# Kernel tuning notes

Hardware: AMD Instinct MI355X
Metric: run time of the kernel (lower is better)

Reference implementation:

```python
import jax, jax.numpy as jnp
import numpy as np

K = 8            # top-k neighbors per channel
BN_EPS = 1e-3    # keras BatchNormalization default


def top_k_features(h, adj, k):
    # h: [N, F], adj: [N, N] (dense). Per node and per channel, take the k
    # largest masked neighbor feature values, then prepend the node's own feature.
    masked = adj[:, None, :] * h.T[None, :, :]        # [N, F, N]
    topk = jax.lax.top_k(masked, k)[0]                # [N, F, K]
    topk = jnp.transpose(topk, (0, 2, 1))             # [N, K, F]
    return jnp.concatenate([h[:, None, :], topk], axis=1)  # [N, K+1, F]


def conv1d(x, w):
    # x: [N, L, Cin], w: [kw, Cin, Cout], VALID 1D conv
    return jax.lax.conv_general_dilated(x, w, (1,), 'VALID',
                                        dimension_numbers=('NWC', 'WIO', 'NWC'))


def batchnorm(x, gamma, beta, mean, var):
    return gamma * (x - mean) * jax.lax.rsqrt(var + BN_EPS) + beta


def setup_inputs():
    key = jax.random.key(0)
    ks = jax.random.split(key, 16)
    N, Fin, H, Cout, NF = 1600, 1433, 32, 7, 8
    x = jax.random.normal(ks[0], (N, Fin), jnp.float32)
    # sparse binary adjacency, avg degree ~16
    adj = (jax.random.uniform(ks[1], (N, N)) < 0.01).astype(jnp.float32)
    mask = jax.random.uniform(ks[2], (N,)) < 0.5

    def g(k, shape, fan_in):
        return jax.random.normal(k, shape, jnp.float32) * (1.0 / np.sqrt(fan_in))

    W0 = g(ks[3], (Fin, H), Fin)                 # DenseConvolution (GCN) weight
    # LGConv block 1: F=32 -> mid (32+8)//2=20 -> 8; kernels 5,5 reduce 9->5->1
    W1a = g(ks[4], (5, 32, 20), 5 * 32)
    W1b = g(ks[5], (5, 20, NF), 5 * 20)
    # LGConv block 2: F=40 -> mid (40+8)//2=24 -> 8
    W2a = g(ks[6], (5, 40, 24), 5 * 40)
    W2b = g(ks[7], (5, 24, NF), 5 * 24)
    Wout = g(ks[8], (H + 2 * NF, Cout), H + 2 * NF)  # 48 -> 7
    bn = {}
    for i, kk in ((1, 9), (2, 12)):
        bn[f'g{i}'] = 1.0 + 0.1 * jax.random.normal(ks[kk], (NF,), jnp.float32)
        bn[f'b{i}'] = 0.1 * jax.random.normal(ks[kk + 1], (NF,), jnp.float32)
        bn[f'm{i}'] = 0.1 * jax.random.normal(ks[kk + 2], (NF,), jnp.float32)
        bn[f'v{i}'] = jax.random.uniform(ks[kk], (NF,), jnp.float32, 0.5, 1.5)
    return {'x': x, 'adj': adj, 'W0': W0, 'W1a': W1a, 'W1b': W1b,
            'W2a': W2a, 'W2b': W2b, 'Wout': Wout,
            'g1': bn['g1'], 'b1': bn['b1'], 'm1': bn['m1'], 'v1': bn['v1'],
            'g2': bn['g2'], 'b2': bn['b2'], 'm2': bn['m2'], 'v2': bn['v2'],
            'mask': mask}


def reference(x, adj, W0, W1a, W1b, W2a, W2b, Wout,
              g1, b1, m1, v1, g2, b2, m2, v2, mask):
    # inference mode: dropout = identity
    h = adj @ (x @ W0)                                # GCN layer, hidden=32
    for Wa, Wb, g, b, m, v in ((W1a, W1b, g1, b1, m1, v1),
                               (W2a, W2b, g2, b2, m2, v2)):
        t = top_k_features(h, adj, K)                 # [N, K+1, F]
        c = conv1d(t, Wa)                             # [N, 5, mid]
        c = conv1d(c, Wb)[:, 0, :]                    # [N, 8]
        c = batchnorm(c, g, b, m, v)
        h = jnp.concatenate([h, c], axis=-1)          # 32 -> 40 -> 48
    logits = adj @ (h @ Wout)                         # [N, 7]
    # Mask layer (boolean_mask); static-shape variant: zero out masked rows
    return jnp.where(mask[:, None], logits, 0.0)
```

## Files before the change

kernel.cpp:

```cpp
#include <hip/hip_runtime.h>


constexpr int NN   = 1600;
constexpr int FIN  = 1433;
constexpr int HGCN = 32;
constexpr int NBS  = 96;
constexpr float BN_EPS = 1e-3f;

constexpr int KS    = 16;
constexpr int CHUNK = 90;
constexpr int BM    = 32;
constexpr int SXS   = 92;
constexpr int RB    = NN / BM;
constexpr int CSRB  = 400;
constexpr int K1B   = CSRB + 1 + RB * KS;
constexpr int GB    = 256;
constexpr int NT    = 512;
constexpr int ZBYTES = 225280;

__device__ __forceinline__ void astore(float* p, float v) {
    __hip_atomic_store(p, v, __ATOMIC_RELAXED, __HIP_MEMORY_SCOPE_AGENT);
}
__device__ __forceinline__ void astorei(int* p, int v) {
    __hip_atomic_store(p, v, __ATOMIC_RELAXED, __HIP_MEMORY_SCOPE_AGENT);
}
__device__ __forceinline__ int aloadi(const int* p) {
    return __hip_atomic_load(p, __ATOMIC_RELAXED, __HIP_MEMORY_SCOPE_AGENT);
}

__global__ __launch_bounds__(512) void zero_k(float4* __restrict__ p) {
    int i = blockIdx.x * 512 + threadIdx.x;
    if (i < ZBYTES / 16) p[i] = make_float4(0.f, 0.f, 0.f, 0.f);
}

__device__ __forceinline__ void gbar(int* cntrel, int phase) {
    int* cnt = cntrel + phase * GB;
    int* rel = cntrel + 896 + phase;
    __syncthreads();
    if (blockIdx.x == 0) {
        int s = threadIdx.x;
        if (s >= 1 && s < GB) {
            while (aloadi(&cnt[s]) == 0) __builtin_amdgcn_s_sleep(1);
        }
        __syncthreads();
        if (threadIdx.x == 0) astorei(rel, 1);
    } else {
        if (threadIdx.x == 0) {
            astorei(&cnt[blockIdx.x], 1);
            while (aloadi(rel) == 0) __builtin_amdgcn_s_sleep(1);
        }
    }
    __syncthreads();
}

__global__ __launch_bounds__(256) void k1(const float* __restrict__ x,
                                          const float* __restrict__ W0,
                                          const float* __restrict__ adj,
                                          const float* __restrict__ W1a,
                                          const float* __restrict__ W2a,
                                          int* __restrict__ deg,
                                          unsigned short* __restrict__ nbr,
                                          const unsigned char* __restrict__ mb,
                                          int* __restrict__ flag,
                                          float* __restrict__ wsT1,
                                          float* __restrict__ wsT2,
                                          float* __restrict__ h0) {
    __shared__ float sx[BM][SXS];
    __shared__ float sw[CHUNK * HGCN];
    int b = blockIdx.x, t = threadIdx.x;

    if (b < CSRB) {
        int lane = t & 63;
        int row  = b * 4 + (t >> 6);
        const float*  ar  = adj + (size_t)row * NN;
        const float4* ar4 = (const float4*)ar;
        unsigned short* nb = nbr + (size_t)row * NBS;
        int cnt = 0;
        #pragma unroll
        for (int it = 0; it < 6; ++it) {
            float4 v = ar4[it * 64 + lane];
            int base = it * 256 + 4 * lane;
            #pragma unroll
            for (int c = 0; c < 4; ++c) {
                float vc = (c == 0) ? v.x : (c == 1) ? v.y : (c == 2) ? v.z : v.w;
                bool p = (vc != 0.0f);
                unsigned long long m = __ballot(p);
                if (p) {
                    int off = cnt + __popcll(m & ((1ull << lane) - 1ull));
                    if (off < NBS) nb[off] = (unsigned short)(base + c);
                }
                cnt += __popcll(m);
            }
        }
        {
            float v = ar[1536 + lane];
            bool p = (v != 0.0f);
            unsigned long long m = __ballot(p);
            if (p) {
                int off = cnt + __popcll(m & ((1ull << lane) - 1ull));
                if (off < NBS) nb[off] = (unsigned short)(1536 + lane);
            }
            cnt += __popcll(m);
        }
        if (lane == 0) deg[row] = cnt < NBS ? cnt : NBS;
        return;
    }

    if (b == CSRB) {
        if (t < 64) {
            int lane = t;
            bool odd = false, flt = false;
            for (int i = lane; i < NN; i += 64) {
                unsigned char v = mb[i];
                if (v) {
                    int r = i & 3;
                    if (r != 0) odd = true;
                    if (r >= 2 && (v == 0x3F || v == 0x80)) flt = true;
                }
            }
            unsigned long long mo = __ballot(odd);
            unsigned long long mf = __ballot(flt);
            if (lane == 0) *flag = mf ? 2 : (mo ? 1 : 0);
        }
        for (int f = t; f < 800; f += 256) {
            int kw = f / 160, r = f - kw * 160, q = r / 20, o = r - q * 20;
            const float* wsrc = W1a + kw * 640 + 4 * q * 20 + o;
            float4 v;
            v.x = wsrc[0]; v.y = wsrc[20]; v.z = wsrc[40]; v.w = wsrc[60];
            ((float4*)wsT1)[f] = v;
        }
        for (int f = t; f < 1200; f += 256) {
            int kw = f / 240, r = f - kw * 240, q = r / 24, o = r - q * 24;
            const float* wsrc = W2a + kw * 960 + 4 * q * 24 + o;
            float4 v;
            v.x = wsrc[0]; v.y = wsrc[24]; v.z = wsrc[48]; v.w = wsrc[72];
            ((float4*)wsT2)[f] = v;
        }
        return;
    }

    int tile = b - (CSRB + 1);
    int rb   = tile % RB;
    int ks   = tile / RB;
    int lane = t & 31;
    int row0 = rb * BM;
    int k0   = ks * CHUNK;
    int vk   = FIN - k0; if (vk > CHUNK) vk = CHUNK;

    {
        int g = t >> 5;
        #pragma unroll
        for (int j = 0; j < 4; ++j) {
            int r = g + 8 * j;
            const float* xr = x + (size_t)(row0 + r) * FIN + k0;
            #pragma unroll
            for (int m = 0; m < 3; ++m) {
                int k = lane + 32 * m;
                if (k < CHUNK) sx[r][k] = (k < vk) ? xr[k] : 0.0f;
            }
        }
    }
    {
        const float4* w4  = (const float4*)(W0 + (size_t)k0 * HGCN);
        float4*       sw4 = (float4*)sw;
        int vf4 = vk * 8;
        for (int i = t; i < CHUNK * 8; i += 256)
            sw4[i] = (i < vf4) ? w4[i] : make_float4(0.f, 0.f, 0.f, 0.f);
    }
    __syncthreads();

    int col = lane;
    int rq  = t >> 5;
    float acc0 = 0.f, acc1 = 0.f, acc2 = 0.f, acc3 = 0.f;
    #pragma unroll 4
    for (int kk = 0; kk < 88; kk += 4) {
        float4 a0 = *(const float4*)&sx[rq     ][kk];
        float4 a1 = *(const float4*)&sx[rq +  8][kk];
        float4 a2 = *(const float4*)&sx[rq + 16][kk];
        float4 a3 = *(const float4*)&sx[rq + 24][kk];
        float w0v = sw[(kk + 0) * HGCN + col];
        float w1v = sw[(kk + 1) * HGCN + col];
        float w2v = sw[(kk + 2) * HGCN + col];
        float w3v = sw[(kk + 3) * HGCN + col];
        acc0 += a0.x * w0v + a0.y * w1v + a0.z * w2v + a0.w * w3v;
        acc1 += a1.x * w0v + a1.y * w1v + a1.z * w2v + a1.w * w3v;
        acc2 += a2.x * w0v + a2.y * w1v + a2.z * w2v + a2.w * w3v;
        acc3 += a3.x * w0v + a3.y * w1v + a3.z * w2v + a3.w * w3v;
    }
    #pragma unroll
    for (int kk = 88; kk < CHUNK; ++kk) {
        float wv = sw[kk * HGCN + col];
        acc0 += sx[rq     ][kk] * wv;
        acc1 += sx[rq +  8][kk] * wv;
        acc2 += sx[rq + 16][kk] * wv;
        acc3 += sx[rq + 24][kk] * wv;
    }

    atomicAdd(&h0[(row0 + rq     ) * HGCN + col], acc0);
    atomicAdd(&h0[(row0 + rq +  8) * HGCN + col], acc1);
    atomicAdd(&h0[(row0 + rq + 16) * HGCN + col], acc2);
    atomicAdd(&h0[(row0 + rq + 24) * HGCN + col], acc3);
}

template<int F, int MID, int TS, bool WRITEZ>
__device__ __forceinline__ void lgconv_phase(int b, int wave, int lane,
        const int* __restrict__ deg, const unsigned short* __restrict__ nbr,
        const float* sWt, const float* __restrict__ Wb,
        const float* __restrict__ g, const float* __restrict__ bb,
        const float* __restrict__ mm, const float* __restrict__ vv,
        const float* __restrict__ h32, const float* __restrict__ c1in,
        const float* __restrict__ Wout,
        float* __restrict__ outbuf, float* T, float* C1, float* sz) {
    int row = b + 256 * wave;
    if (row >= NN) return;
    int d = deg[row];
    const unsigned short* nb = nbr + (size_t)row * NBS;

    if (lane < F) {
        float t0=0.f,t1=0.f,t2=0.f,t3=0.f,t4=0.f,t5=0.f,t6=0.f,t7=0.f;
        #define BUBBLE(val_) { float val=val_, c;                       \
            c = t0; t0 = fmaxf(c, val); val = fminf(c, val);            \
            c = t1; t1 = fmaxf(c, val); val = fminf(c, val);            \
            c = t2; t2 = fmaxf(c, val); val = fminf(c, val);            \
            c = t3; t3 = fmaxf(c, val); val = fminf(c, val);            \
            c = t4; t4 = fmaxf(c, val); val = fminf(c, val);            \
            c = t5; t5 = fmaxf(c, val); val = fminf(c, val);            \
            c = t6; t6 = fmaxf(c, val); val = fminf(c, val);            \
            c = t7; t7 = fmaxf(c, val); val = fminf(c, val); }
        #define LDV(n_) ((F == 32) ? h32[(n_) * HGCN + lane]            \
            : ((lane < 32) ? h32[(n_) * HGCN + lane] : c1in[(n_) * 8 + (lane - 32)]))
        int it = 0;
        for (; it + 8 <= d; it += 8) {
            float v[8];
            #pragma unroll
            for (int j = 0; j < 8; ++j) v[j] = LDV((int)nb[it + j]);
            #pragma unroll
            for (int j = 0; j < 8; ++j) BUBBLE(v[j]);
        }
        for (; it < d; ++it) BUBBLE(LDV((int)nb[it]));
        T[0*TS+lane] = LDV(row);
        T[1*TS+lane] = t0; T[2*TS+lane] = t1; T[3*TS+lane] = t2; T[4*TS+lane] = t3;
        T[5*TS+lane] = t4; T[6*TS+lane] = t5; T[7*TS+lane] = t6; T[8*TS+lane] = t7;
        #undef LDV
        #undef BUBBLE
    }
    for (int oi = lane; oi < 5 * MID; oi += 64) {
        int p = oi / MID, o = oi - p * MID;
        float ax = 0.f, ay = 0.f, az = 0.f, aw = 0.f;
        #pragma unroll
        for (int kw = 0; kw < 5; ++kw) {
            const float4* t4 = (const float4*)&T[(p + kw) * TS];
            const float4* w4 = ((const float4*)sWt) + kw * (F / 4) * MID + o;
            #pragma unroll
            for (int q = 0; q < F / 4; ++q) {
                float4 tv = t4[q], wv = w4[q * MID];
                ax += tv.x * wv.x; ay += tv.y * wv.y;
                az += tv.z * wv.z; aw += tv.w * wv.w;
            }
        }
        C1[p * MID + o] = (ax + ay) + (az + aw);
    }
    if (lane < 8) {
        float acc = 0.f;
        #pragma unroll
        for (int kw = 0; kw < 5; ++kw)
            for (int ci = 0; ci < MID; ++ci)
                acc += C1[kw * MID + ci] * Wb[(kw * MID + ci) * 8 + lane];
        float y = g[lane] * (acc - mm[lane]) * rsqrtf(vv[lane] + BN_EPS) + bb[lane];
        if (WRITEZ) sz[lane] = y;
        else        astore(&outbuf[row * 8 + lane], y);
    }
    if (WRITEZ) {
        if (lane < 8) {
            float z = 0.f;
            if (lane < 7) {
                #pragma unroll
                for (int k = 0; k < 40; ++k) z += T[k] * Wout[k * 7 + lane];
                #pragma unroll
                for (int j = 0; j < 8; ++j)  z += sz[j] * Wout[(40 + j) * 7 + lane];
            }
            astore(&outbuf[row * 8 + lane], z);
        }
    }
}

__global__ __launch_bounds__(NT) void k2(
        const int* __restrict__ deg, const unsigned short* __restrict__ nbr,
        const float* __restrict__ h0,
        float* __restrict__ h32, float* __restrict__ c1, float* __restrict__ zbuf,
        const float* __restrict__ wsT1, const float* __restrict__ wsT2,
        const float* __restrict__ W1b,
        const float* __restrict__ g1, const float* __restrict__ b1,
        const float* __restrict__ m1, const float* __restrict__ v1,
        const float* __restrict__ W2b,
        const float* __restrict__ g2, const float* __restrict__ b2,
        const float* __restrict__ m2, const float* __restrict__ v2,
        const float* __restrict__ Wout, const void* __restrict__ mask,
        const int* __restrict__ flag, int* __restrict__ cntrel,
        float* __restrict__ out) {
    __shared__ float sWt1[3200];
    __shared__ float sWt2[4800];
    __shared__ float T   [8][400];
    __shared__ float C1s [8][120];
    __shared__ float szs [8][8];
    int t = threadIdx.x, b = blockIdx.x;
    int wave = t >> 6, lane = t & 63;

    {
        const float4* s1 = (const float4*)wsT1;
        const float4* s2 = (const float4*)wsT2;
        float4* d1 = (float4*)sWt1;
        float4* d2 = (float4*)sWt2;
        for (int i = t; i < 800;  i += NT) d1[i] = s1[i];
        for (int i = t; i < 1200; i += NT) d2[i] = s2[i];
    }

    {
        int row = b + 256 * wave;
        if (row < NN) {
            int f = lane & 31, half = lane >> 5;
            int d = deg[row];
            const unsigned short* nb = nbr + (size_t)row * NBS;
            float acc = 0.f;
            int it = half;
            for (; it + 16 <= d; it += 16) {
                float v[8];
                #pragma unroll
                for (int j = 0; j < 8; ++j) v[j] = h0[(int)nb[it + 2 * j] * HGCN + f];
                #pragma unroll
                for (int j = 0; j < 8; ++j) acc += v[j];
            }
            for (; it < d; it += 2) acc += h0[(int)nb[it] * HGCN + f];
            acc += __shfl_xor(acc, 32);
            if (half == 0) astore(&h32[row * HGCN + f], acc);
        }
    }
    gbar(cntrel, 0);

    lgconv_phase<32, 20, 36, false>(b, wave, lane, deg, nbr, sWt1, W1b,
                                    g1, b1, m1, v1, h32, nullptr, Wout, c1,
                                    T[wave], C1s[wave], szs[wave]);
    gbar(cntrel, 1);

    lgconv_phase<40, 24, 44, true>(b, wave, lane, deg, nbr, sWt2, W2b,
                                   g2, b2, m2, v2, h32, c1, Wout, zbuf,
                                   T[wave], C1s[wave], szs[wave]);
    gbar(cntrel, 2);

    {
        int row = b + 256 * wave;
        if (row < NN) {
            int d = deg[row];
            const unsigned short* nb = nbr + (size_t)row * NBS;
            int ng = lane >> 3, c = lane & 7;
            float acc = 0.f;
            for (int it = ng; it < d; it += 8)
                acc += zbuf[(int)nb[it] * 8 + c];
            acc += __shfl_xor(acc, 8);
            acc += __shfl_xor(acc, 16);
            acc += __shfl_xor(acc, 32);
            if (lane < 7) {
                int fl = *flag;
                bool mk;
                if (fl == 2)      mk = ((const float*)mask)[row] != 0.0f;
                else if (fl == 1) mk = ((const unsigned char*)mask)[row] != 0;
                else              mk = ((const int*)mask)[row] != 0;
                out[row * 7 + lane] = mk ? acc : 0.0f;
            }
        }
    }
}

extern "C" void kernel_launch(void* const* d_in, const int* in_sizes, int n_in,
                              void* d_out, int out_size, void* d_ws, size_t ws_size,
                              hipStream_t stream) {
    const float* x    = (const float*)d_in[0];
    const float* adj  = (const float*)d_in[1];
    const float* W0   = (const float*)d_in[2];
    const float* W1a  = (const float*)d_in[3];
    const float* W1b  = (const float*)d_in[4];
    const float* W2a  = (const float*)d_in[5];
    const float* W2b  = (const float*)d_in[6];
    const float* Wout = (const float*)d_in[7];
    const float* g1 = (const float*)d_in[8];
    const float* b1 = (const float*)d_in[9];
    const float* m1 = (const float*)d_in[10];
    const float* v1 = (const float*)d_in[11];
    const float* g2 = (const float*)d_in[12];
    const float* b2 = (const float*)d_in[13];
    const float* m2 = (const float*)d_in[14];
    const float* v2 = (const float*)d_in[15];
    const void*  mask = d_in[16];

    char* ws = (char*)d_ws;
    int*            cntrel = (int*)(ws + 0);
    float*          h0     = (float*)(ws + 20480);
    int*            flag   = (int*)(ws + 225280);
    int*            deg    = (int*)(ws + 225792);
    unsigned short* nbr    = (unsigned short*)(ws + 232192);
    float*          h32    = (float*)(ws + 539392);
    float*          c1     = (float*)(ws + 744192);
    float*          zbuf   = (float*)(ws + 795392);
    float*          wsT1   = (float*)(ws + 846592);
    float*          wsT2   = (float*)(ws + 859392);

    float* out = (float*)d_out;

    zero_k<<<(ZBYTES / 16 + 511) / 512, 512, 0, stream>>>((float4*)ws);
    k1<<<K1B, 256, 0, stream>>>(x, W0, adj, W1a, W2a, deg, nbr,
                                (const unsigned char*)mask, flag, wsT1, wsT2, h0);
    k2<<<GB, NT, 0, stream>>>(deg, nbr, h0, h32, c1, zbuf, wsT1, wsT2,
                              W1b, g1, b1, m1, v1,
                              W2b, g2, b2, m2, v2,
                              Wout, mask, flag, cntrel, out);
}
```

Measured before the change: 50.60 us.

## Reuse block-1 top-k rows in block 2 and restructure LGConv convolutions

In block 2, the top-k selection for the first 32 channels is no longer recomputed. Only the 8 new channels are sorted, and the block-1 results kept in each wave's shared T buffer are reused, since that buffer now uses a common stride for both blocks. The first conv is register-blocked so each lane computes all 5 output positions from shared T loads, and the second conv weights are staged in LDS. The second conv is spread across all 64 lanes with a shuffle reduction instead of 8 serial lanes. This relies on T persisting per wave across the grid barriers with the same row mapping.

Result: faster. 48.42 us (median of 2 runs) (-4.3%).

```diff
diff --git a/kernel.cpp b/kernel.cpp
--- a/kernel.cpp
+++ b/kernel.cpp
@@ -16,6 +16,7 @@
 constexpr int K1B   = CSRB + 1 + RB * KS;
 constexpr int GB    = 256;
 constexpr int NT    = 512;
+constexpr int TS    = 44;
 constexpr int ZBYTES = 225280;
 
 __device__ __forceinline__ void astore(float* p, float v) {
@@ -202,21 +203,22 @@
     atomicAdd(&h0[(row0 + rq + 24) * HGCN + col], acc3);
 }
 
-template<int F, int MID, int TS, bool WRITEZ>
+template<int F, int MID, bool WRITEZ>
 __device__ __forceinline__ void lgconv_phase(int b, int wave, int lane,
         const int* __restrict__ deg, const unsigned short* __restrict__ nbr,
-        const float* sWt, const float* __restrict__ Wb,
+        const float* sWt, const float* sWb,
         const float* __restrict__ g, const float* __restrict__ bb,
         const float* __restrict__ mm, const float* __restrict__ vv,
         const float* __restrict__ h32, const float* __restrict__ c1in,
         const float* __restrict__ Wout,
-        float* __restrict__ outbuf, float* T, float* C1, float* sz) {
+        float* __restrict__ outbuf, float* T, float* C1) {
     int row = b + 256 * wave;
     if (row >= NN) return;
     int d = deg[row];
     const unsigned short* nb = nbr + (size_t)row * NBS;
 
-    if (lane < F) {
+    bool tk = (F == 32) ? (lane < 32) : (lane >= 32 && lane < 40);
+    if (tk) {
         float t0=0.f,t1=0.f,t2=0.f,t3=0.f,t4=0.f,t5=0.f,t6=0.f,t7=0.f;
         #define BUBBLE(val_) { float val=val_, c;                       \
             c = t0; t0 = fmaxf(c, val); val = fminf(c, val);            \
@@ -228,7 +230,7 @@
             c = t6; t6 = fmaxf(c, val); val = fminf(c, val);            \
             c = t7; t7 = fmaxf(c, val); val = fminf(c, val); }
         #define LDV(n_) ((F == 32) ? h32[(n_) * HGCN + lane]            \
-            : ((lane < 32) ? h32[(n_) * HGCN + lane] : c1in[(n_) * 8 + (lane - 32)]))
+                                   : c1in[(n_) * 8 + (lane - 32)])
         int it = 0;
         for (; it + 8 <= d; it += 8) {
             float v[8];
@@ -244,42 +246,68 @@
         #undef LDV
         #undef BUBBLE
     }
-    for (int oi = lane; oi < 5 * MID; oi += 64) {
-        int p = oi / MID, o = oi - p * MID;
-        float ax = 0.f, ay = 0.f, az = 0.f, aw = 0.f;
-        #pragma unroll
-        for (int kw = 0; kw < 5; ++kw) {
-            const float4* t4 = (const float4*)&T[(p + kw) * TS];
-            const float4* w4 = ((const float4*)sWt) + kw * (F / 4) * MID + o;
-            #pragma unroll
-            for (int q = 0; q < F / 4; ++q) {
-                float4 tv = t4[q], wv = w4[q * MID];
-                ax += tv.x * wv.x; ay += tv.y * wv.y;
-                az += tv.z * wv.z; aw += tv.w * wv.w;
-            }
-        }
-        C1[p * MID + o] = (ax + ay) + (az + aw);
-    }
-    if (lane < 8) {
+
+    if (lane < MID) {
+        int o = lane;
+        float4 a0 = {0,0,0,0}, a1 = {0,0,0,0}, a2 = {0,0,0,0},
+               a3 = {0,0,0,0}, a4 = {0,0,0,0};
+        for (int q = 0; q < F / 4; ++q) {
+            float4 tq[9];
+            #pragma unroll
+            for (int pos = 0; pos < 9; ++pos)
+                tq[pos] = *(const float4*)&T[pos * TS + 4 * q];
+            #pragma unroll
+            for (int kw = 0; kw < 5; ++kw) {
+                float4 wv = ((const float4*)sWt)[(kw * (F / 4) + q) * MID + o];
+                #define ACC(ap_, pos_) { float4 tv = tq[pos_];          \
+                    ap_.x += tv.x * wv.x; ap_.y += tv.y * wv.y;         \
+                    ap_.z += tv.z * wv.z; ap_.w += tv.w * wv.w; }
+                ACC(a0, kw + 0) ACC(a1, kw + 1) ACC(a2, kw + 2)
+                ACC(a3, kw + 3) ACC(a4, kw + 4)
+                #undef ACC
+            }
+        }
+        C1[0 * MID + o] = (a0.x + a0.y) + (a0.z + a0.w);
+        C1[1 * MID + o] = (a1.x + a1.y) + (a1.z + a1.w);
+        C1[2 * MID + o] = (a2.x + a2.y) + (a2.z + a2.w);
+        C1[3 * MID + o] = (a3.x + a3.y) + (a3.z + a3.w);
+        C1[4 * MID + o] = (a4.x + a4.y) + (a4.z + a4.w);
+    }
+
+    {
+        int grp = lane >> 3, o = lane & 7;
         float acc = 0.f;
-        #pragma unroll
-        for (int kw = 0; kw < 5; ++kw)
-            for (int ci = 0; ci < MID; ++ci)
-                acc += C1[kw * MID + ci] * Wb[(kw * MID + ci) * 8 + lane];
-        float y = g[lane] * (acc - mm[lane]) * rsqrtf(vv[lane] + BN_EPS) + bb[lane];
-        if (WRITEZ) sz[lane] = y;
-        else        astore(&outbuf[row * 8 + lane], y);
-    }
-    if (WRITEZ) {
-        if (lane < 8) {
-            float z = 0.f;
-            if (lane < 7) {
-                #pragma unroll
-                for (int k = 0; k < 40; ++k) z += T[k] * Wout[k * 7 + lane];
-                #pragma unroll
-                for (int j = 0; j < 8; ++j)  z += sz[j] * Wout[(40 + j) * 7 + lane];
-            }
-            astore(&outbuf[row * 8 + lane], z);
+        for (int idx = grp; idx < 5 * MID; idx += 8)
+            acc += C1[idx] * sWb[idx * 8 + o];
+        acc += __shfl_xor(acc, 8);
+        acc += __shfl_xor(acc, 16);
+        acc += __shfl_xor(acc, 32);
+        float y = g[o] * (acc - mm[o]) * rsqrtf(vv[o] + BN_EPS) + bb[o];
+
+        if (!WRITEZ) {
+            if (lane < 8) astore(&outbuf[row * 8 + lane], y);
+        } else {
+            float yv[8];
+            #pragma unroll
+            for (int j = 0; j < 8; ++j) yv[j] = __shfl(y, j);
+            if (lane < 8) {
+                float z = 0.f;
+                if (lane < 7) {
+                    const float4* tf = (const float4*)T;
+                    #pragma unroll
+                    for (int k4 = 0; k4 < 10; ++k4) {
+                        float4 tv = tf[k4];
+                        z += tv.x * Wout[(4 * k4 + 0) * 7 + lane]
+                           + tv.y * Wout[(4 * k4 + 1) * 7 + lane]
+                           + tv.z * Wout[(4 * k4 + 2) * 7 + lane]
+                           + tv.w * Wout[(4 * k4 + 3) * 7 + lane];
+                    }
+                    #pragma unroll
+                    for (int j = 0; j < 8; ++j)
+                        z += yv[j] * Wout[(40 + j) * 7 + lane];
+                }
+                astore(&outbuf[row * 8 + lane], z);
+            }
         }
     }
 }
@@ -300,19 +328,26 @@
         float* __restrict__ out) {
     __shared__ float sWt1[3200];
     __shared__ float sWt2[4800];
-    __shared__ float T   [8][400];
+    __shared__ float sWb1[800];
+    __shared__ float sWb2[960];
+    __shared__ float T   [8][9 * TS + 4];
     __shared__ float C1s [8][120];
-    __shared__ float szs [8][8];
     int t = threadIdx.x, b = blockIdx.x;
     int wave = t >> 6, lane = t & 63;
 
     {
         const float4* s1 = (const float4*)wsT1;
         const float4* s2 = (const float4*)wsT2;
+        const float4* s3 = (const float4*)W1b;
+        const float4* s4 = (const float4*)W2b;
         float4* d1 = (float4*)sWt1;
         float4* d2 = (float4*)sWt2;
+        float4* d3 = (float4*)sWb1;
+        float4* d4 = (float4*)sWb2;
         for (int i = t; i < 800;  i += NT) d1[i] = s1[i];
         for (int i = t; i < 1200; i += NT) d2[i] = s2[i];
+        for (int i = t; i < 200;  i += NT) d3[i] = s3[i];
+        for (int i = t; i < 240;  i += NT) d4[i] = s4[i];
     }
 
     {
@@ -337,14 +372,14 @@
     }
     gbar(cntrel, 0);
 
-    lgconv_phase<32, 20, 36, false>(b, wave, lane, deg, nbr, sWt1, W1b,
-                                    g1, b1, m1, v1, h32, nullptr, Wout, c1,
-                                    T[wave], C1s[wave], szs[wave]);
+    lgconv_phase<32, 20, false>(b, wave, lane, deg, nbr, sWt1, sWb1,
+                                g1, b1, m1, v1, h32, nullptr, Wout, c1,
+                                T[wave], C1s[wave]);
     gbar(cntrel, 1);
 
-    lgconv_phase<40, 24, 44, true>(b, wave, lane, deg, nbr, sWt2, W2b,
-                                   g2, b2, m2, v2, h32, c1, Wout, zbuf,
-                                   T[wave], C1s[wave], szs[wave]);
+    lgconv_phase<40, 24, true>(b, wave, lane, deg, nbr, sWt2, sWb2,
+                               g2, b2, m2, v2, h32, c1, Wout, zbuf,
+                               T[wave], C1s[wave]);
     gbar(cntrel, 2);
 
     {
```
